# Optimization experiments

Measured on AMD Instinct MI355X. Metric: run time of the kernel, lower is better.

The kernel has to match this reference:

```python
import jax, jax.numpy as jnp
import numpy as np

WS, SS, NH = 7, 3, 16  # window_size, shift_size, num_heads


def _rel_pos_index(ws):
    coords = np.stack(np.meshgrid(np.arange(ws), np.arange(ws), indexing='ij'))  # (2, ws, ws)
    cf = coords.reshape(2, -1)                       # (2, N)
    rel = (cf[:, :, None] - cf[:, None, :]).transpose(1, 2, 0).copy()  # (N, N, 2)
    rel[:, :, 0] += ws - 1
    rel[:, :, 1] += ws - 1
    rel[:, :, 0] *= 2 * ws - 1
    return rel.sum(-1)                               # (N, N) int indices into bias table


def _attn_mask(Hp, Wp, ws, ss):
    img = np.zeros((Hp, Wp))
    slices = (slice(0, -ws), slice(-ws, -ss), slice(-ss, None))
    cnt = 0
    for h in slices:
        for w in slices:
            img[h, w] = cnt
            cnt += 1
    mw = img.reshape(Hp // ws, ws, Wp // ws, ws).transpose(0, 2, 1, 3).reshape(-1, ws * ws)  # (nW, N)
    am = mw[:, None, :] - mw[:, :, None]             # (nW, N, N)
    return np.where(am != 0, -100.0, 0.0).astype(np.float32)


def setup_inputs() -> dict:
    key = jax.random.key(0)
    k1, k2, k3, k4 = jax.random.split(key, 4)
    B, H, W, C = 16, 56, 56, 512
    return {
        'q_out': jax.random.normal(k1, (B, H, W, C), dtype=jnp.float32),
        'k_out': jax.random.normal(k2, (B, H, W, C), dtype=jnp.float32),
        'v_out': jax.random.normal(k3, (B, H, W, C), dtype=jnp.float32),
        'bias_table': 0.02 * jax.random.normal(k4, ((2 * WS - 1) ** 2, NH), dtype=jnp.float32),
        'C': C, 'H': H, 'W': W,
        'x_low_padding_h': 0, 'x_low_padding_w': 0,
    }


def reference(q_out, k_out, v_out, bias_table, C, H, W, x_low_padding_h, x_low_padding_w):
    ws, ss, nh = WS, SS, NH
    Hp, Wp = H + x_low_padding_h, W + x_low_padding_w
    B = q_out.shape[0]
    hd = C // nh
    scale = hd ** (-0.5)
    N = ws * ws

    def part(x):  # (B,Hp,Wp,C) -> (B*nW, N, C)
        x = x.reshape(B, Hp // ws, ws, Wp // ws, ws, C).transpose(0, 1, 3, 2, 4, 5)
        return x.reshape(-1, N, C)

    # cyclic shift
    sq = jnp.roll(q_out, (-ss, -ss), axis=(1, 2))
    sk = jnp.roll(k_out, (-ss, -ss), axis=(1, 2))
    sv = jnp.roll(v_out, (-ss, -ss), axis=(1, 2))

    qw, kw, vw = part(sq), part(sk), part(sv)
    B_ = qw.shape[0]
    q = qw.reshape(B_, N, nh, hd).transpose(0, 2, 1, 3) * scale  # (B_, nh, N, hd)
    k = kw.reshape(B_, N, nh, hd).transpose(0, 2, 1, 3)
    v = vw.reshape(B_, N, nh, hd).transpose(0, 2, 1, 3)

    attn = jnp.einsum('bhnd,bhmd->bhnm', q, k)  # (B_, nh, N, N)

    # relative position bias
    rpi = _rel_pos_index(ws)
    bias = bias_table[rpi.reshape(-1)].reshape(N, N, nh).transpose(2, 0, 1)  # (nh, N, N)
    attn = attn + bias[None]

    # shift mask
    am = jnp.asarray(_attn_mask(Hp, Wp, ws, ss), dtype=attn.dtype)  # (nW, N, N)
    nW = am.shape[0]
    attn = attn.reshape(B_ // nW, nW, nh, N, N) + am[None, :, None]
    attn = jax.nn.softmax(attn.reshape(B_, nh, N, N), axis=-1)

    xw = jnp.einsum('bhnm,bhmd->bhnd', attn, v).transpose(0, 2, 1, 3).reshape(B_, N, C)

    # window reverse + reverse shift
    x = xw.reshape(B, Hp // ws, Wp // ws, ws, ws, C).transpose(0, 1, 3, 2, 4, 5).reshape(B, Hp, Wp, C)
    return jnp.roll(x, (ss, ss), axis=(1, 2))
```

## Files before the change

kernel.cpp:

```cpp
#include <hip/hip_runtime.h>
#include <stdint.h>


constexpr int WSZ  = 7;
constexpr int NTOK = 49;
constexpr int NH_  = 16;
constexpr int HD_  = 32;
constexpr int SP   = 56;
constexpr int CH   = 512;
constexpr float LOG2E = 1.4426950408889634f;

typedef float    f32x4 __attribute__((ext_vector_type(4)));
typedef short    s16x8 __attribute__((ext_vector_type(8)));
typedef _Float16 f16x4 __attribute__((ext_vector_type(4)));

union FragU { uint32_t w[4]; s16x8 v; };

__device__ __forceinline__ uint32_t bf16_hibits(float x) {
    uint32_t u = __float_as_uint(x);
    u += 0x7fffu + ((u >> 16) & 1u);
    return u & 0xffff0000u;
}
__device__ __forceinline__ uint32_t pk_bf16(float a, float b) {
    return (bf16_hibits(a) >> 16) | bf16_hibits(b);
}

__device__ __forceinline__ void ld128x2(const float* p, float4& lo, float4& hi) {
    asm volatile("global_load_dwordx4 %0, %2, off\n\t"
                 "global_load_dwordx4 %1, %2, off offset:16"
                 : "=&v"(lo), "=&v"(hi) : "v"(p) : "memory");
}
__device__ __forceinline__ void ld32x2(const float* p, float& a, float& b) {
    asm volatile("global_load_dword %0, %2, off\n\t"
                 "global_load_dword %1, %2, off offset:64"
                 : "=&v"(a), "=&v"(b) : "v"(p) : "memory");
}
__device__ __forceinline__ void fence_vmem() {
    asm volatile("s_waitcnt vmcnt(0)" ::: "memory");
    __builtin_amdgcn_sched_barrier(0);
}

__global__ __launch_bounds__(256)
void build_bm(const float* __restrict__ bias, _Float16* __restrict__ bm)
{
    const int blk = blockIdx.x;
    const int h = blk >> 2, cls = blk & 3;
    for (int idx = threadIdx.x; idx < 4096; idx += 256) {
        const int q = idx >> 6, m = idx & 63;
        float val;
        if (q >= NTOK || m >= NTOK) {
            val = -1000.0f;
        } else {
            const int iq = q / 7, jq = q % 7, im = m / 7, jm = m % 7;
            const int rpi = (iq - im + 6) * 13 + (jq - jm + 6);
            const float bv = bias[rpi * NH_ + h];
            const int rq = ((cls & 2) ? (iq < 4 ? 3 : 6) : 0)
                         + ((cls & 1) ? (jq < 4 ? 1 : 2) : 0);
            const int rm = ((cls & 2) ? (im < 4 ? 3 : 6) : 0)
                         + ((cls & 1) ? (jm < 4 ? 1 : 2) : 0);
            const float mask = (rq != rm) ? -100.0f : 0.0f;
            val = (bv + mask) * LOG2E;
        }
        bm[blk * 4096 + idx] = (_Float16)val;
    }
}

__global__ __launch_bounds__(256, 2)
void swin_mfma_kernel(const float* __restrict__ qg,
                      const float* __restrict__ kg,
                      const float* __restrict__ vg,
                      const _Float16* __restrict__ bm,
                      float* __restrict__ outg)
{
    const int wave = threadIdx.x >> 6;
    const int wh   = blockIdx.x * 4 + wave;
    const int h    = wh & (NH_ - 1);
    const int w    = wh >> 4;
    const int wc   = w & 7;
    const int wr   = (w >> 3) & 7;
    const int b    = w >> 6;

    const int lane = threadIdx.x & 63;
    const int g    = lane >> 4;
    const int l16  = lane & 15;

    const int t  = lane < NTOK ? lane : NTOK - 1;
    const int it = t / 7, jt = t - 7 * it;
    int sr = wr * 7 + it + 3; if (sr >= SP) sr -= SP;
    int sc = wc * 7 + jt + 3; if (sc >= SP) sc -= SP;
    const int off_t = ((b * SP + sr) * SP + sc) * CH + h * HD_;

    int oQK[4];
#pragma unroll
    for (int tt = 0; tt < 4; ++tt) oQK[tt] = __shfl(off_t, 16 * tt + l16);
    int oV[16];
#pragma unroll
    for (int mc = 0; mc < 2; ++mc)
#pragma unroll
        for (int e = 0; e < 8; ++e) oV[8 * mc + e] = __shfl(off_t, 32 * mc + 8 * g + e);

    const int cls = ((wr == 7) ? 2 : 0) | ((wc == 7) ? 1 : 0);
    const _Float16* bmh = bm + ((size_t)h * 4 + cls) * 4096;

    float4 qa[4][2], ka[4][2];
#pragma unroll
    for (int tt = 0; tt < 4; ++tt)
        ld128x2(qg + oQK[tt] + 8 * g, qa[tt][0], qa[tt][1]);
#pragma unroll
    for (int tt = 0; tt < 4; ++tt)
        ld128x2(kg + oQK[tt] + 8 * g, ka[tt][0], ka[tt][1]);
    float va[2][2][8];
#pragma unroll
    for (int mc = 0; mc < 2; ++mc)
#pragma unroll
        for (int e = 0; e < 8; ++e)
            ld32x2(vg + oV[8 * mc + e] + l16, va[mc][0][e], va[mc][1][e]);

    f16x4 bmr[4][4];
#pragma unroll
    for (int tq = 0; tq < 4; ++tq)
#pragma unroll
        for (int tk = 0; tk < 4; ++tk)
            bmr[tq][tk] = *(const f16x4*)(bmh + (16 * tq + l16) * 64 + 16 * tk + 4 * g);

    fence_vmem();

    const float qs = 0.17677669529663687f * LOG2E;

    s16x8 Qh[4], Kh[4], Vb[2][2];
#pragma unroll
    for (int tt = 0; tt < 4; ++tt) {
        FragU qh, kh;
        qh.w[0] = pk_bf16(qa[tt][0].x * qs, qa[tt][0].y * qs);
        qh.w[1] = pk_bf16(qa[tt][0].z * qs, qa[tt][0].w * qs);
        qh.w[2] = pk_bf16(qa[tt][1].x * qs, qa[tt][1].y * qs);
        qh.w[3] = pk_bf16(qa[tt][1].z * qs, qa[tt][1].w * qs);
        kh.w[0] = pk_bf16(ka[tt][0].x, ka[tt][0].y);
        kh.w[1] = pk_bf16(ka[tt][0].z, ka[tt][0].w);
        kh.w[2] = pk_bf16(ka[tt][1].x, ka[tt][1].y);
        kh.w[3] = pk_bf16(ka[tt][1].z, ka[tt][1].w);
        Qh[tt] = qh.v; Kh[tt] = kh.v;
    }
#pragma unroll
    for (int mc = 0; mc < 2; ++mc)
#pragma unroll
        for (int dh = 0; dh < 2; ++dh) {
            FragU fu;
#pragma unroll
            for (int wd = 0; wd < 4; ++wd)
                fu.w[wd] = pk_bf16(va[mc][dh][2 * wd], va[mc][dh][2 * wd + 1]);
            Vb[mc][dh] = fu.v;
        }

    uint32_t u0[4][4], u1[4][4];
    float inv[4];
#pragma unroll
    for (int tq = 0; tq < 4; ++tq) {
        float dsum = 0.f;
#pragma unroll
        for (int tk = 0; tk < 4; ++tk) {
            f32x4 a;
            a[0] = (float)bmr[tq][tk][0] - 23.f;
            a[1] = (float)bmr[tq][tk][1] - 23.f;
            a[2] = (float)bmr[tq][tk][2] - 23.f;
            a[3] = (float)bmr[tq][tk][3] - 23.f;
            a = __builtin_amdgcn_mfma_f32_16x16x32_bf16(Kh[tk], Qh[tq], a, 0, 0, 0);
            float e0 = __builtin_amdgcn_exp2f(a[0]);
            float e1 = __builtin_amdgcn_exp2f(a[1]);
            float e2 = __builtin_amdgcn_exp2f(a[2]);
            float e3 = __builtin_amdgcn_exp2f(a[3]);
            dsum += (e0 + e1) + (e2 + e3);
            u0[tq][tk] = pk_bf16(e0, e1);
            u1[tq][tk] = pk_bf16(e2, e3);
        }
        dsum += __shfl_xor(dsum, 16);
        dsum += __shfl_xor(dsum, 32);
        inv[tq] = 1.0f / (dsum + 1e-30f);
    }

    const int srcb = 32 * (g & 1) + l16;
    const bool hiG = (lane >= 32);
    s16x8 PA[4][2];
#pragma unroll
    for (int tq = 0; tq < 4; ++tq)
#pragma unroll
        for (int mc = 0; mc < 2; ++mc) {
            FragU fu;
#pragma unroll
            for (int wd = 0; wd < 4; ++wd) {
                const int sl = srcb + 16 * (wd >> 1);
                uint32_t A, B;
                if (wd & 1) {
                    A = __shfl(u1[tq][2 * mc],     sl);
                    B = __shfl(u1[tq][2 * mc + 1], sl);
                } else {
                    A = __shfl(u0[tq][2 * mc],     sl);
                    B = __shfl(u0[tq][2 * mc + 1], sl);
                }
                fu.w[wd] = hiG ? B : A;
            }
            PA[tq][mc] = fu.v;
        }

#pragma unroll
    for (int tq = 0; tq < 4; ++tq) {
        const float iv = inv[tq];
        const bool ok = (tq < 3) || (l16 == 0);
#pragma unroll
        for (int dh = 0; dh < 2; ++dh) {
            f32x4 a = {0.f, 0.f, 0.f, 0.f};
            a = __builtin_amdgcn_mfma_f32_16x16x32_bf16(Vb[0][dh], PA[tq][0], a, 0, 0, 0);
            a = __builtin_amdgcn_mfma_f32_16x16x32_bf16(Vb[1][dh], PA[tq][1], a, 0, 0, 0);
            if (ok) {
                float4 st;
                st.x = a[0] * iv; st.y = a[1] * iv;
                st.z = a[2] * iv; st.w = a[3] * iv;
                *(float4*)(outg + oQK[tq] + 16 * dh + 4 * g) = st;
            }
        }
    }
}

__global__ __launch_bounds__(256)
void swin_block_scalar(const float* __restrict__ qg,
                       const float* __restrict__ kg,
                       const float* __restrict__ vg,
                       const float* __restrict__ bias,
                       float* __restrict__ outg)
{
    const int wave = __builtin_amdgcn_readfirstlane(threadIdx.x >> 6);
    const int wh   = blockIdx.x * 4 + wave;
    const int h    = wh & (NH_ - 1);
    const int w    = wh >> 4;
    const int wc   = w & 7;
    const int wr   = (w >> 3) & 7;
    const int b    = w >> 6;

    const int lane = threadIdx.x & 63;
    const int rr   = lane < NTOK ? lane : NTOK - 1;
    const int i    = rr / WSZ;
    const int j    = rr - i * WSZ;

    const int hp = wr * WSZ + i;
    const int wp = wc * WSZ + j;
    int sr = hp + 3; if (sr >= SP) sr -= SP;
    int sc = wp + 3; if (sc >= SP) sc -= SP;
    const int rowoff = ((b * SP + sr) * SP + sc) * CH + h * HD_;
    const int reg_r = (hp < 49 ? 0 : (hp < 53 ? 3 : 6))
                    + (wp < 49 ? 0 : (wp < 53 ? 1 : 2));
    const float qscale = 0.17677669529663687f * LOG2E;

    float qr[HD_];
    {
        const float4* qp = reinterpret_cast<const float4*>(qg + rowoff);
#pragma unroll
        for (int tt = 0; tt < HD_ / 4; ++tt) {
            float4 x = qp[tt];
            qr[4*tt+0] = x.x * qscale; qr[4*tt+1] = x.y * qscale;
            qr[4*tt+2] = x.z * qscale; qr[4*tt+3] = x.w * qscale;
        }
    }
    const int biaslane = (i * 13 + j) * 16 + h;
    float o[HD_];
#pragma unroll
    for (int d = 0; d < HD_; ++d) o[d] = 0.f;
    float denom = 0.f;
    const float* kb = kg + b * SP * SP * CH + h * HD_;
    const float* vb = vg + b * SP * SP * CH + h * HD_;

    for (int ic = 0; ic < WSZ; ++ic) {
        const int hpc = wr * WSZ + ic;
        int src_r = hpc + 3; if (src_r >= SP) src_r -= SP;
        const int regh_c = (hpc < 49 ? 0 : (hpc < 53 ? 3 : 6));
        const float* krow0 = kb + src_r * SP * CH;
        const float* vrow0 = vb + src_r * SP * CH;
        float e[WSZ];
#pragma unroll
        for (int u = 0; u < WSZ; ++u) {
            const int wpc = wc * WSZ + u;
            int src_c = wpc + 3; if (src_c >= SP) src_c -= SP;
            const int reg_c = regh_c + (wpc < 49 ? 0 : (wpc < 53 ? 1 : 2));
            const float* krow = krow0 + src_c * CH;
            const float bv = bias[biaslane + ((6 - ic) * 13 + (6 - u)) * 16];
            float s0 = fmaf(bv, LOG2E, (reg_r != reg_c) ? -167.26950408889634f : -23.0f);
            float s1 = 0.f, s2 = 0.f, s3 = 0.f;
#pragma unroll
            for (int d = 0; d < HD_; d += 4) {
                s0 = fmaf(qr[d+0], krow[d+0], s0);
                s1 = fmaf(qr[d+1], krow[d+1], s1);
                s2 = fmaf(qr[d+2], krow[d+2], s2);
                s3 = fmaf(qr[d+3], krow[d+3], s3);
            }
            e[u] = exp2f((s0 + s1) + (s2 + s3));
            denom += e[u];
        }
#pragma unroll
        for (int u = 0; u < WSZ; ++u) {
            const int wpc = wc * WSZ + u;
            int src_c = wpc + 3; if (src_c >= SP) src_c -= SP;
            const float* vrow = vrow0 + src_c * CH;
            const float ev = e[u];
#pragma unroll
            for (int d = 0; d < HD_; ++d) o[d] = fmaf(ev, vrow[d], o[d]);
        }
    }
    const float invd = 1.0f / denom;
    if (lane < NTOK) {
        float4* op = reinterpret_cast<float4*>(outg + rowoff);
#pragma unroll
        for (int tt = 0; tt < HD_ / 4; ++tt) {
            float4 x;
            x.x = o[4*tt+0] * invd; x.y = o[4*tt+1] * invd;
            x.z = o[4*tt+2] * invd; x.w = o[4*tt+3] * invd;
            op[tt] = x;
        }
    }
}

extern "C" void kernel_launch(void* const* d_in, const int* in_sizes, int n_in,
                              void* d_out, int out_size, void* d_ws, size_t ws_size,
                              hipStream_t stream) {
    const float* q    = (const float*)d_in[0];
    const float* k    = (const float*)d_in[1];
    const float* v    = (const float*)d_in[2];
    const float* bias = (const float*)d_in[3];
    float* out        = (float*)d_out;

    const int B   = in_sizes[0] / (SP * SP * CH);
    const int nwh = B * (SP / WSZ) * (SP / WSZ) * NH_;

    const size_t bm_bytes = (size_t)NH_ * 4 * 4096 * sizeof(_Float16);
    if (ws_size >= bm_bytes) {
        _Float16* bm = (_Float16*)d_ws;
        hipLaunchKernelGGL(build_bm, dim3(NH_ * 4), dim3(256), 0, stream, bias, bm);
        hipLaunchKernelGGL(swin_mfma_kernel, dim3(nwh / 4), dim3(256), 0, stream,
                           q, k, v, bm, out);
    } else {
        hipLaunchKernelGGL(swin_block_scalar, dim3(nwh / 4), dim3(256), 0, stream,
                           q, k, v, bias, out);
    }
}
```

Measured before the change: 101.8 us.

## Process two window-heads per wave with prefetch of second window's loads

Refactors the MFMA attention kernel into helpers and has each wave handle two window-heads, half the grid apart. Global loads for the second window are issued before the softmax/MFMA math of the first, so memory latency overlaps compute. The grid shrinks by half and register use grows for the extra prefetch buffers, which may lower occupancy.

```diff
diff --git a/kernel.cpp b/kernel.cpp
--- a/kernel.cpp
+++ b/kernel.cpp
@@ -65,69 +65,53 @@
     }
 }
 
-__global__ __launch_bounds__(256, 2)
-void swin_mfma_kernel(const float* __restrict__ qg,
-                      const float* __restrict__ kg,
-                      const float* __restrict__ vg,
-                      const _Float16* __restrict__ bm,
-                      float* __restrict__ outg)
-{
-    const int wave = threadIdx.x >> 6;
-    const int wh   = blockIdx.x * 4 + wave;
-    const int h    = wh & (NH_ - 1);
-    const int w    = wh >> 4;
-    const int wc   = w & 7;
-    const int wr   = (w >> 3) & 7;
-    const int b    = w >> 6;
-
-    const int lane = threadIdx.x & 63;
-    const int g    = lane >> 4;
-    const int l16  = lane & 15;
-
+struct Frag { s16x8 Qh[4], Kh[4], Vb[2][2]; };
+
+__device__ __forceinline__ int make_off(int wh, int lane) {
+    const int h  = wh & 15;
+    const int w  = wh >> 4;
+    const int wc = w & 7, wr = (w >> 3) & 7, b = w >> 6;
     const int t  = lane < NTOK ? lane : NTOK - 1;
     const int it = t / 7, jt = t - 7 * it;
     int sr = wr * 7 + it + 3; if (sr >= SP) sr -= SP;
     int sc = wc * 7 + jt + 3; if (sc >= SP) sc -= SP;
-    const int off_t = ((b * SP + sr) * SP + sc) * CH + h * HD_;
-
-    int oQK[4];
-#pragma unroll
-    for (int tt = 0; tt < 4; ++tt) oQK[tt] = __shfl(off_t, 16 * tt + l16);
+    return ((b * SP + sr) * SP + sc) * CH + h * HD_;
+}
+__device__ __forceinline__ int cls_of(int wh) {
+    const int w = wh >> 4;
+    return ((((w >> 3) & 7) == 7) ? 2 : 0) | (((w & 7) == 7) ? 1 : 0);
+}
+
+__device__ __forceinline__ void issue_asm(const float* __restrict__ qg,
+                                          const float* __restrict__ kg,
+                                          const float* __restrict__ vg,
+                                          int off, int l16, int g,
+                                          float4 (&qa)[4][2], float4 (&ka)[4][2],
+                                          float (&va)[2][2][8], int (&oQK)[4]) {
+#pragma unroll
+    for (int tt = 0; tt < 4; ++tt) oQK[tt] = __shfl(off, 16 * tt + l16);
     int oV[16];
 #pragma unroll
     for (int mc = 0; mc < 2; ++mc)
 #pragma unroll
-        for (int e = 0; e < 8; ++e) oV[8 * mc + e] = __shfl(off_t, 32 * mc + 8 * g + e);
-
-    const int cls = ((wr == 7) ? 2 : 0) | ((wc == 7) ? 1 : 0);
-    const _Float16* bmh = bm + ((size_t)h * 4 + cls) * 4096;
-
-    float4 qa[4][2], ka[4][2];
+        for (int e = 0; e < 8; ++e) oV[8 * mc + e] = __shfl(off, 32 * mc + 8 * g + e);
 #pragma unroll
     for (int tt = 0; tt < 4; ++tt)
         ld128x2(qg + oQK[tt] + 8 * g, qa[tt][0], qa[tt][1]);
 #pragma unroll
     for (int tt = 0; tt < 4; ++tt)
         ld128x2(kg + oQK[tt] + 8 * g, ka[tt][0], ka[tt][1]);
-    float va[2][2][8];
 #pragma unroll
     for (int mc = 0; mc < 2; ++mc)
 #pragma unroll
         for (int e = 0; e < 8; ++e)
             ld32x2(vg + oV[8 * mc + e] + l16, va[mc][0][e], va[mc][1][e]);
-
-    f16x4 bmr[4][4];
-#pragma unroll
-    for (int tq = 0; tq < 4; ++tq)
-#pragma unroll
-        for (int tk = 0; tk < 4; ++tk)
-            bmr[tq][tk] = *(const f16x4*)(bmh + (16 * tq + l16) * 64 + 16 * tk + 4 * g);
-
-    fence_vmem();
-
-    const float qs = 0.17677669529663687f * LOG2E;
-
-    s16x8 Qh[4], Kh[4], Vb[2][2];
+}
+
+__device__ __forceinline__ void convert_all(const float4 (&qa)[4][2],
+                                            const float4 (&ka)[4][2],
+                                            const float (&va)[2][2][8],
+                                            float qs, Frag& f) {
 #pragma unroll
     for (int tt = 0; tt < 4; ++tt) {
         FragU qh, kh;
@@ -139,7 +123,7 @@
         kh.w[1] = pk_bf16(ka[tt][0].z, ka[tt][0].w);
         kh.w[2] = pk_bf16(ka[tt][1].x, ka[tt][1].y);
         kh.w[3] = pk_bf16(ka[tt][1].z, ka[tt][1].w);
-        Qh[tt] = qh.v; Kh[tt] = kh.v;
+        f.Qh[tt] = qh.v; f.Kh[tt] = kh.v;
     }
 #pragma unroll
     for (int mc = 0; mc < 2; ++mc)
@@ -149,9 +133,22 @@
 #pragma unroll
             for (int wd = 0; wd < 4; ++wd)
                 fu.w[wd] = pk_bf16(va[mc][dh][2 * wd], va[mc][dh][2 * wd + 1]);
-            Vb[mc][dh] = fu.v;
-        }
-
+            f.Vb[mc][dh] = fu.v;
+        }
+}
+
+__device__ __forceinline__ void load_bm(const _Float16* __restrict__ bmh,
+                                        int l16, int g, f16x4 (&bmr)[4][4]) {
+#pragma unroll
+    for (int tq = 0; tq < 4; ++tq)
+#pragma unroll
+        for (int tk = 0; tk < 4; ++tk)
+            bmr[tq][tk] = *(const f16x4*)(bmh + (16 * tq + l16) * 64 + 16 * tk + 4 * g);
+}
+
+__device__ __forceinline__ void do_math(const Frag& f, const f16x4 (&bmr)[4][4],
+                                        const int (&oQK)[4], int lane, int g, int l16,
+                                        float* __restrict__ outg) {
     uint32_t u0[4][4], u1[4][4];
     float inv[4];
 #pragma unroll
@@ -164,7 +161,7 @@
             a[1] = (float)bmr[tq][tk][1] - 23.f;
             a[2] = (float)bmr[tq][tk][2] - 23.f;
             a[3] = (float)bmr[tq][tk][3] - 23.f;
-            a = __builtin_amdgcn_mfma_f32_16x16x32_bf16(Kh[tk], Qh[tq], a, 0, 0, 0);
+            a = __builtin_amdgcn_mfma_f32_16x16x32_bf16(f.Kh[tk], f.Qh[tq], a, 0, 0, 0);
             float e0 = __builtin_amdgcn_exp2f(a[0]);
             float e1 = __builtin_amdgcn_exp2f(a[1]);
             float e2 = __builtin_amdgcn_exp2f(a[2]);
@@ -180,9 +177,9 @@
 
     const int srcb = 32 * (g & 1) + l16;
     const bool hiG = (lane >= 32);
-    s16x8 PA[4][2];
-#pragma unroll
-    for (int tq = 0; tq < 4; ++tq)
+#pragma unroll
+    for (int tq = 0; tq < 4; ++tq) {
+        s16x8 PA0, PA1;
 #pragma unroll
         for (int mc = 0; mc < 2; ++mc) {
             FragU fu;
@@ -199,18 +196,15 @@
                 }
                 fu.w[wd] = hiG ? B : A;
             }
-            PA[tq][mc] = fu.v;
-        }
-
-#pragma unroll
-    for (int tq = 0; tq < 4; ++tq) {
+            if (mc == 0) PA0 = fu.v; else PA1 = fu.v;
+        }
         const float iv = inv[tq];
         const bool ok = (tq < 3) || (l16 == 0);
 #pragma unroll
         for (int dh = 0; dh < 2; ++dh) {
             f32x4 a = {0.f, 0.f, 0.f, 0.f};
-            a = __builtin_amdgcn_mfma_f32_16x16x32_bf16(Vb[0][dh], PA[tq][0], a, 0, 0, 0);
-            a = __builtin_amdgcn_mfma_f32_16x16x32_bf16(Vb[1][dh], PA[tq][1], a, 0, 0, 0);
+            a = __builtin_amdgcn_mfma_f32_16x16x32_bf16(f.Vb[0][dh], PA0, a, 0, 0, 0);
+            a = __builtin_amdgcn_mfma_f32_16x16x32_bf16(f.Vb[1][dh], PA1, a, 0, 0, 0);
             if (ok) {
                 float4 st;
                 st.x = a[0] * iv; st.y = a[1] * iv;
@@ -219,6 +213,51 @@
             }
         }
     }
+}
+
+__global__ __launch_bounds__(256, 2)
+void swin_d2asm_kernel(const float* __restrict__ qg,
+                       const float* __restrict__ kg,
+                       const float* __restrict__ vg,
+                       const _Float16* __restrict__ bm,
+                       float* __restrict__ outg, int whStep)
+{
+    const int wave = threadIdx.x >> 6;
+    const int gw   = blockIdx.x * 4 + wave;
+    const int lane = threadIdx.x & 63;
+    const int g    = lane >> 4;
+    const int l16  = lane & 15;
+    const float qs = 0.17677669529663687f * LOG2E;
+
+    const int h = gw & 15;
+    const _Float16* bmhead = bm + (size_t)h * 4 * 4096;
+
+    const int wh0 = gw, wh1 = gw + whStep;
+
+    float4 qa[4][2], ka[4][2];
+    float  va[2][2][8];
+    int oQK0[4];
+    issue_asm(qg, kg, vg, make_off(wh0, lane), l16, g, qa, ka, va, oQK0);
+    f16x4 bmr[4][4];
+    load_bm(bmhead + cls_of(wh0) * 4096, l16, g, bmr);
+    fence_vmem();
+
+    Frag f;
+    convert_all(qa, ka, va, qs, f);
+
+    float4 qb[4][2], kb[4][2];
+    float  vb[2][2][8];
+    int oQK1[4];
+    issue_asm(qg, kg, vg, make_off(wh1, lane), l16, g, qb, kb, vb, oQK1);
+    __builtin_amdgcn_sched_barrier(0);
+
+    do_math(f, bmr, oQK0, lane, g, l16, outg);
+
+    fence_vmem();
+    convert_all(qb, kb, vb, qs, f);
+    load_bm(bmhead + cls_of(wh1) * 4096, l16, g, bmr);
+    __builtin_amdgcn_sched_barrier(0);
+    do_math(f, bmr, oQK1, lane, g, l16, outg);
 }
 
 __global__ __launch_bounds__(256)
@@ -330,11 +369,11 @@
     const int nwh = B * (SP / WSZ) * (SP / WSZ) * NH_;
 
     const size_t bm_bytes = (size_t)NH_ * 4 * 4096 * sizeof(_Float16);
-    if (ws_size >= bm_bytes) {
+    if (ws_size >= bm_bytes && (nwh % 8) == 0) {
         _Float16* bm = (_Float16*)d_ws;
         hipLaunchKernelGGL(build_bm, dim3(NH_ * 4), dim3(256), 0, stream, bias, bm);
-        hipLaunchKernelGGL(swin_mfma_kernel, dim3(nwh / 4), dim3(256), 0, stream,
-                           q, k, v, bm, out);
+        hipLaunchKernelGGL(swin_d2asm_kernel, dim3(nwh / 8), dim3(256), 0, stream,
+                           q, k, v, bm, out, nwh / 2);
     } else {
         hipLaunchKernelGGL(swin_block_scalar, dim3(nwh / 4), dim3(256), 0, stream,
                            q, k, v, bias, out);
```

Result: slower. 107.7 us (+5.8%).
